# Kernel tuning notes

Hardware: AMD Instinct MI355X
Metric: run time of the kernel (lower is better)

The kernel has to match this reference:

```python
import jax, jax.numpy as jnp
import numpy as np

EMBED_DIM = 384
NUM_HEADS = 6
HEAD_DIM = EMBED_DIM // NUM_HEADS
SCALE = HEAD_DIM ** -0.5


def setup_inputs() -> dict:
    key = jax.random.key(0)
    k_x, k_qkv_w, k_qkv_b, k_p_w, k_p_b = jax.random.split(key, 5)
    B, N, C = 8, 2048, EMBED_DIM
    x = jax.random.normal(k_x, (B, N, C), dtype=jnp.float32)
    # nn.Linear init ~ U(-1/sqrt(fan_in), 1/sqrt(fan_in)); scaled normal is fine for a reference
    s = 1.0 / np.sqrt(C)
    qkv_w = jax.random.uniform(k_qkv_w, (C, 3 * C), minval=-s, maxval=s, dtype=jnp.float32)
    qkv_b = jax.random.uniform(k_qkv_b, (3 * C,), minval=-s, maxval=s, dtype=jnp.float32)
    proj_w = jax.random.uniform(k_p_w, (C, C), minval=-s, maxval=s, dtype=jnp.float32)
    proj_b = jax.random.uniform(k_p_b, (C,), minval=-s, maxval=s, dtype=jnp.float32)
    return {"x": x, "qkv_w": qkv_w, "qkv_b": qkv_b, "proj_w": proj_w, "proj_b": proj_b}


def reference(x, qkv_w, qkv_b, proj_w, proj_b):
    B, N, C = x.shape
    H, D = NUM_HEADS, C // NUM_HEADS
    qkv = x @ qkv_w + qkv_b                      # [B, N, 3C]
    qkv = qkv.reshape(B, N, 3, H, D)
    q = qkv[:, :, 0].transpose(0, 2, 1, 3)       # [B, H, N, D]
    k = qkv[:, :, 1].transpose(0, 2, 1, 3)
    v = qkv[:, :, 2].transpose(0, 2, 1, 3)
    attn = jnp.einsum('bhnd,bhmd->bhnm', q, k) * SCALE  # [B, H, N, N]
    attn = jax.nn.softmax(attn, axis=-1)
    out = jnp.einsum('bhnm,bhmd->bhnd', attn, v)        # [B, H, N, D]
    out = out.transpose(0, 2, 1, 3).reshape(B, N, C)
    return out @ proj_w + proj_b
```

## Files before the change

### kernel.cpp

```cpp
#include <hip/hip_runtime.h>
#include <hip/hip_bf16.h>
#include <stdint.h>

#define NUM_HEADS 6
#define HEAD_DIM  64
#define EMB       384
#define SEQ       2048
#define NBATCH    8
#define NBH       48
#define QKV_COLS  1152
#define ROWS      16384
#define L2E       1.44269504f

typedef __attribute__((ext_vector_type(8))) short bf16x8;
typedef __attribute__((ext_vector_type(4))) short bf16x4;
typedef __attribute__((ext_vector_type(4))) float f32x4;

typedef const __attribute__((address_space(1))) void gas_void;
typedef __attribute__((address_space(3))) void las_void;

static __device__ __forceinline__ short f2bf(float f) {
    __hip_bfloat16 h = __float2bfloat16(f);
    return __builtin_bit_cast(short, h);
}

__global__ void xcvt_kernel(const float* __restrict__ in, short* __restrict__ out) {
    int i = (blockIdx.x * 256 + threadIdx.x) * 8;
    f32x4 a = *(const f32x4*)&in[i];
    f32x4 b = *(const f32x4*)&in[i + 4];
    bf16x8 o;
    o[0] = f2bf(a[0]); o[1] = f2bf(a[1]); o[2] = f2bf(a[2]); o[3] = f2bf(a[3]);
    o[4] = f2bf(b[0]); o[5] = f2bf(b[1]); o[6] = f2bf(b[2]); o[7] = f2bf(b[3]);
    *(bf16x8*)&out[i] = o;
}

__global__ void wtrans_kernel(const float* __restrict__ in, short* __restrict__ out,
                              int rows, int cols) {
    __shared__ float tile[32][33];
    int c0 = blockIdx.x * 32, r0 = blockIdx.y * 32;
    int x = threadIdx.x, y = threadIdx.y;
#pragma unroll
    for (int i = 0; i < 32; i += 8)
        tile[y + i][x] = in[(size_t)(r0 + y + i) * cols + c0 + x];
    __syncthreads();
#pragma unroll
    for (int i = 0; i < 32; i += 8)
        out[(size_t)(c0 + y + i) * rows + r0 + x] = f2bf(tile[x][y + i]);
}

#define BM 128
#define BN 128
#define BK 64
#define LDP 80

__global__ __launch_bounds__(256, 2) void qkv_gemm_kernel(
    const short* __restrict__ Xb, const short* __restrict__ WT,
    const float* __restrict__ bias,
    short* __restrict__ Qb, short* __restrict__ Kb, short* __restrict__ Vt)
{
    __shared__ short At[BM][LDP];
    __shared__ short Bt[BN][LDP];
    const int orig = blockIdx.x;
    const int wgid = (orig & 7) * 144 + (orig >> 3);
    const int m0 = (wgid / 9) * BM;
    const int n0 = (wgid % 9) * BN;
    const int tid = threadIdx.x;
    const int lane = tid & 63, wid = tid >> 6;
    const int wm = wid >> 1, wn = wid & 1;
    const int lr = lane & 15, lg = lane >> 4;
    f32x4 acc[4][4] = {};

    for (int k0 = 0; k0 < EMB; k0 += BK) {
        int r = tid >> 3, c = (tid & 7) * 8;
#pragma unroll
        for (int i = 0; i < 4; ++i)
            *(bf16x8*)&At[r + i * 32][c] = *(const bf16x8*)&Xb[(size_t)(m0 + r + i * 32) * EMB + k0 + c];
#pragma unroll
        for (int i = 0; i < 4; ++i)
            *(bf16x8*)&Bt[r + i * 32][c] = *(const bf16x8*)&WT[(size_t)(n0 + r + i * 32) * EMB + k0 + c];
        __syncthreads();
#pragma unroll
        for (int kk = 0; kk < 2; ++kk) {
            bf16x8 af[4], bg[4];
#pragma unroll
            for (int mi = 0; mi < 4; ++mi)
                af[mi] = *(const bf16x8*)&At[wm * 64 + mi * 16 + lr][kk * 32 + lg * 8];
#pragma unroll
            for (int ni = 0; ni < 4; ++ni)
                bg[ni] = *(const bf16x8*)&Bt[wn * 64 + ni * 16 + lr][kk * 32 + lg * 8];
#pragma unroll
            for (int mi = 0; mi < 4; ++mi)
#pragma unroll
                for (int ni = 0; ni < 4; ++ni)
                    acc[mi][ni] = __builtin_amdgcn_mfma_f32_16x16x32_bf16(af[mi], bg[ni], acc[mi][ni], 0, 0, 0);
        }
        __syncthreads();
    }
    const int mat = n0 / EMB;
#pragma unroll
    for (int ni = 0; ni < 4; ++ni) {
        int col = n0 + wn * 64 + ni * 16 + lr;
        float bv = bias[col];
        int rem = col - mat * EMB;
        int h = rem >> 6, d = rem & 63;
#pragma unroll
        for (int mi = 0; mi < 4; ++mi) {
#pragma unroll
            for (int j = 0; j < 4; ++j) {
                int row = m0 + wm * 64 + mi * 16 + lg * 4 + j;
                int b = row >> 11, n = row & 2047;
                float v = acc[mi][ni][j] + bv;
                size_t bh = (size_t)(b * NUM_HEADS + h);
                if (mat == 0)      Qb[(bh * SEQ + n) * HEAD_DIM + d] = f2bf(v * (0.125f * L2E));
                else if (mat == 1) Kb[(bh * SEQ + n) * HEAD_DIM + d] = f2bf(v);
                else               Vt[(bh * HEAD_DIM + d) * SEQ + n] = f2bf(v);
            }
        }
    }
}

__global__ __launch_bounds__(256, 4) void attn_kernel(
    const short* __restrict__ Qb, const short* __restrict__ Kb,
    const short* __restrict__ Vg, short* __restrict__ AO)
{
    __shared__ alignas(16) char Kl[2][8192];
    __shared__ alignas(16) char Vl[2][8192];
    __shared__ alignas(16) char Pl[4][2048];

    const int orig = blockIdx.x;
    const int wgid = (orig & 7) * 96 + (orig >> 3);
    const int bh = wgid >> 4;
    const int qb = wgid & 15;
    const int tid = threadIdx.x, lane = tid & 63, wid = tid >> 6;
    const int lr = lane & 15, lg = lane >> 4;
    const int q0 = qb * 128 + wid * 32;
    const short* Qh = Qb + (size_t)bh * SEQ * HEAD_DIM;
    const char*  Khc = (const char*)(Kb + (size_t)bh * SEQ * HEAD_DIM);
    const char*  Vhc = (const char*)(Vg + (size_t)bh * HEAD_DIM * SEQ);

    const int s_r0 = wid * 16 + (lane >> 3);
    const int s_cb0 = ((lane & 7) * 16) ^ ((s_r0 & 7) << 4);
    const int s_r1 = s_r0 + 8;
    const int s_cb1 = ((lane & 7) * 16) ^ ((s_r1 & 7) << 4);

#define STAGE(buf, kbase)                                                               \
    do {                                                                                \
        __builtin_amdgcn_global_load_lds(                                               \
            (gas_void*)(Khc + ((size_t)(kbase) + s_r0) * 128 + s_cb0),                  \
            (las_void*)(&Kl[buf][wid * 2048]), 16, 0, 0);                               \
        __builtin_amdgcn_global_load_lds(                                               \
            (gas_void*)(Khc + ((size_t)(kbase) + s_r1) * 128 + s_cb1),                  \
            (las_void*)(&Kl[buf][wid * 2048 + 1024]), 16, 0, 0);                        \
        __builtin_amdgcn_global_load_lds(                                               \
            (gas_void*)(Vhc + (size_t)s_r0 * (SEQ * 2) + (size_t)(kbase) * 2 + s_cb0),  \
            (las_void*)(&Vl[buf][wid * 2048]), 16, 0, 0);                               \
        __builtin_amdgcn_global_load_lds(                                               \
            (gas_void*)(Vhc + (size_t)s_r1 * (SEQ * 2) + (size_t)(kbase) * 2 + s_cb1),  \
            (las_void*)(&Vl[buf][wid * 2048 + 1024]), 16, 0, 0);                        \
    } while (0)

    bf16x8 qf[2][2];
#pragma unroll
    for (int c2 = 0; c2 < 2; ++c2)
#pragma unroll
        for (int kk = 0; kk < 2; ++kk)
            qf[c2][kk] = *(const bf16x8*)&Qh[(size_t)(q0 + c2 * 16 + lr) * HEAD_DIM + kk * 32 + lg * 8];

    bf16x8 ones;
#pragma unroll
    for (int e = 0; e < 8; ++e) ones[e] = (short)0x3F80;

    f32x4 acc[2][4] = {};
    f32x4 accl[2] = {};

    char* const PlW = Pl[wid];
    const int swp = (lr & 7) << 4;

    STAGE(0, 0);
    __syncthreads();

    for (int t = 0; t < SEQ / 64; ++t) {
        const int cur = t & 1;
        if (t + 1 < SEQ / 64) STAGE(cur ^ 1, (t + 1) * 64);

        const char* Kt = Kl[cur];
        const char* Vt_ = Vl[cur];

        f32x4 s[2][4] = {};
        __builtin_amdgcn_s_setprio(1);
#pragma unroll
        for (int c = 0; c < 4; ++c) {
            const int row = c * 16 + lr;
            const int sw = (row & 7) << 4;
            bf16x8 k0 = *(const bf16x8*)(Kt + row * 128 + ((lg * 16) ^ sw));
            bf16x8 k1 = *(const bf16x8*)(Kt + row * 128 + ((64 + lg * 16) ^ sw));
            s[0][c] = __builtin_amdgcn_mfma_f32_16x16x32_bf16(k0, qf[0][0], s[0][c], 0, 0, 0);
            s[0][c] = __builtin_amdgcn_mfma_f32_16x16x32_bf16(k1, qf[0][1], s[0][c], 0, 0, 0);
            s[1][c] = __builtin_amdgcn_mfma_f32_16x16x32_bf16(k0, qf[1][0], s[1][c], 0, 0, 0);
            s[1][c] = __builtin_amdgcn_mfma_f32_16x16x32_bf16(k1, qf[1][1], s[1][c], 0, 0, 0);
        }
        __builtin_amdgcn_s_setprio(0);

        bf16x8 pb[2][2];
#pragma unroll
        for (int c2 = 0; c2 < 2; ++c2) {
#pragma unroll
            for (int c = 0; c < 4; ++c) {
                bf16x4 q4;
#pragma unroll
                for (int j = 0; j < 4; ++j)
                    q4[j] = f2bf(__builtin_amdgcn_exp2f(s[c2][c][j]));
                *(bf16x4*)(PlW + lr * 128 + ((c * 32 + lg * 8) ^ swp)) = q4;
            }
#pragma unroll
            for (int kk = 0; kk < 2; ++kk)
                pb[c2][kk] = *(const bf16x8*)(PlW + lr * 128 + ((kk * 64 + lg * 16) ^ swp));
        }

        __builtin_amdgcn_s_setprio(1);
#pragma unroll
        for (int f = 0; f < 4; ++f) {
            const int row = f * 16 + lr;
            const int sw = (row & 7) << 4;
            bf16x8 v0 = *(const bf16x8*)(Vt_ + row * 128 + ((lg * 16) ^ sw));
            bf16x8 v1 = *(const bf16x8*)(Vt_ + row * 128 + ((64 + lg * 16) ^ sw));
            acc[0][f] = __builtin_amdgcn_mfma_f32_16x16x32_bf16(v0, pb[0][0], acc[0][f], 0, 0, 0);
            acc[0][f] = __builtin_amdgcn_mfma_f32_16x16x32_bf16(v1, pb[0][1], acc[0][f], 0, 0, 0);
            acc[1][f] = __builtin_amdgcn_mfma_f32_16x16x32_bf16(v0, pb[1][0], acc[1][f], 0, 0, 0);
            acc[1][f] = __builtin_amdgcn_mfma_f32_16x16x32_bf16(v1, pb[1][1], acc[1][f], 0, 0, 0);
        }
        accl[0] = __builtin_amdgcn_mfma_f32_16x16x32_bf16(ones, pb[0][0], accl[0], 0, 0, 0);
        accl[0] = __builtin_amdgcn_mfma_f32_16x16x32_bf16(ones, pb[0][1], accl[0], 0, 0, 0);
        accl[1] = __builtin_amdgcn_mfma_f32_16x16x32_bf16(ones, pb[1][0], accl[1], 0, 0, 0);
        accl[1] = __builtin_amdgcn_mfma_f32_16x16x32_bf16(ones, pb[1][1], accl[1], 0, 0, 0);
        __builtin_amdgcn_s_setprio(0);

        __syncthreads();
    }
#undef STAGE

    const int b = bh / NUM_HEADS, h = bh - b * NUM_HEADS;
#pragma unroll
    for (int c2 = 0; c2 < 2; ++c2) {
        const float inv = 1.f / accl[c2][0];
        const size_t rowbase = ((size_t)(b * SEQ + q0 + c2 * 16 + lr)) * EMB + h * HEAD_DIM;
#pragma unroll
        for (int f = 0; f < 4; ++f) {
            bf16x4 o4;
#pragma unroll
            for (int j = 0; j < 4; ++j)
                o4[j] = f2bf(acc[c2][f][j] * inv);
            *(bf16x4*)&AO[rowbase + f * 16 + lg * 4] = o4;
        }
    }
}

__global__ __launch_bounds__(256, 2) void proj_gemm_kernel(
    const short* __restrict__ Ain, const short* __restrict__ WT,
    const float* __restrict__ bias, float* __restrict__ Out)
{
    __shared__ short At[64][LDP];
    __shared__ short Bt[128][LDP];
    const int orig = blockIdx.x;
    const int idx = orig >> 3;
    const int m0 = ((orig & 7) * 32 + idx / 3) * 64;
    const int n0 = (idx % 3) * 128;
    const int tid = threadIdx.x;
    const int lane = tid & 63, wid = tid >> 6;
    const int wm = wid >> 1, wn = wid & 1;
    const int lr = lane & 15, lg = lane >> 4;
    f32x4 acc[2][4] = {};

    for (int k0 = 0; k0 < EMB; k0 += BK) {
        int r = tid >> 3, c = (tid & 7) * 8;
#pragma unroll
        for (int i = 0; i < 2; ++i)
            *(bf16x8*)&At[r + i * 32][c] = *(const bf16x8*)&Ain[(size_t)(m0 + r + i * 32) * EMB + k0 + c];
#pragma unroll
        for (int i = 0; i < 4; ++i)
            *(bf16x8*)&Bt[r + i * 32][c] = *(const bf16x8*)&WT[(size_t)(n0 + r + i * 32) * EMB + k0 + c];
        __syncthreads();
#pragma unroll
        for (int kk = 0; kk < 2; ++kk) {
            bf16x8 af[2], bg[4];
#pragma unroll
            for (int mi = 0; mi < 2; ++mi)
                af[mi] = *(const bf16x8*)&At[wm * 32 + mi * 16 + lr][kk * 32 + lg * 8];
#pragma unroll
            for (int ni = 0; ni < 4; ++ni)
                bg[ni] = *(const bf16x8*)&Bt[wn * 64 + ni * 16 + lr][kk * 32 + lg * 8];
#pragma unroll
            for (int mi = 0; mi < 2; ++mi)
#pragma unroll
                for (int ni = 0; ni < 4; ++ni)
                    acc[mi][ni] = __builtin_amdgcn_mfma_f32_16x16x32_bf16(af[mi], bg[ni], acc[mi][ni], 0, 0, 0);
        }
        __syncthreads();
    }
#pragma unroll
    for (int ni = 0; ni < 4; ++ni) {
        int col = n0 + wn * 64 + ni * 16 + lr;
        float bv = bias[col];
#pragma unroll
        for (int mi = 0; mi < 2; ++mi)
#pragma unroll
            for (int j = 0; j < 4; ++j) {
                int row = m0 + wm * 32 + mi * 16 + lg * 4 + j;
                Out[(size_t)row * EMB + col] = acc[mi][ni][j] + bv;
            }
    }
}

extern "C" void kernel_launch(void* const* d_in, const int* in_sizes, int n_in,
                              void* d_out, int out_size, void* d_ws, size_t ws_size,
                              hipStream_t stream) {
    const float* x      = (const float*)d_in[0];
    const float* qkv_w  = (const float*)d_in[1];
    const float* qkv_b  = (const float*)d_in[2];
    const float* proj_w = (const float*)d_in[3];
    const float* proj_b = (const float*)d_in[4];
    float* out = (float*)d_out;

    char* ws = (char*)d_ws;
    short* qkv_wT  = (short*)(ws);
    short* proj_wT = (short*)(ws + 884736);
    short* Qb      = (short*)(ws + 1179648);
    short* Kb      = (short*)(ws + 13762560);
    short* Vt      = (short*)(ws + 26345472);
    short* AOXb    = (short*)(ws + 38928384);

    wtrans_kernel<<<dim3(QKV_COLS / 32, EMB / 32), dim3(32, 8), 0, stream>>>(qkv_w, qkv_wT, EMB, QKV_COLS);
    wtrans_kernel<<<dim3(EMB / 32, EMB / 32), dim3(32, 8), 0, stream>>>(proj_w, proj_wT, EMB, EMB);
    xcvt_kernel<<<dim3(ROWS * EMB / 8 / 256), 256, 0, stream>>>(x, AOXb);
    qkv_gemm_kernel<<<dim3(ROWS / BM * (QKV_COLS / BN)), 256, 0, stream>>>(AOXb, qkv_wT, qkv_b, Qb, Kb, Vt);
    attn_kernel<<<dim3(NBH * (SEQ / 128)), 256, 0, stream>>>(Qb, Kb, Vt, AOXb);
    proj_gemm_kernel<<<dim3(ROWS / 64 * (EMB / 128)), 256, 0, stream>>>(AOXb, proj_wT, proj_b, out);
}
```

Measured before the change: 138.4 us.

## Double-buffer GEMM tiles via direct global-to-LDS loads with XOR swizzle

Both the QKV and projection GEMMs now load tiles with global_load_lds into double-buffered, XOR-swizzled shared memory, prefetching the next K-tile while MFMAs run on the current one. Wave priority is raised around the MFMA loop. The V output, previously written with strided scalar stores into the transposed Vt, is now transposed through LDS and written as contiguous 16-byte vectors. The proj kernel's occupancy hint rises to 3; the larger LDS footprint and the extra barrier in the V epilogue are the trade-offs.

```diff
diff --git a/kernel.cpp b/kernel.cpp
--- a/kernel.cpp
+++ b/kernel.cpp
@@ -51,15 +51,13 @@
 #define BM 128
 #define BN 128
 #define BK 64
-#define LDP 80
 
 __global__ __launch_bounds__(256, 2) void qkv_gemm_kernel(
     const short* __restrict__ Xb, const short* __restrict__ WT,
     const float* __restrict__ bias,
     short* __restrict__ Qb, short* __restrict__ Kb, short* __restrict__ Vt)
 {
-    __shared__ short At[BM][LDP];
-    __shared__ short Bt[BN][LDP];
+    __shared__ alignas(16) char smem[2][32768];
     const int orig = blockIdx.x;
     const int wgid = (orig & 7) * 144 + (orig >> 3);
     const int m0 = (wgid / 9) * BM;
@@ -68,54 +66,105 @@
     const int lane = tid & 63, wid = tid >> 6;
     const int wm = wid >> 1, wn = wid & 1;
     const int lr = lane & 15, lg = lane >> 4;
+    const char* Xc = (const char*)Xb;
+    const char* Wc = (const char*)WT;
+
+    const int t_r = wid * 32 + (lane >> 3);
+    const int t_cb = ((lane & 7) * 16) ^ (((lane >> 3) & 7) << 4);
+
+#define GSTAGE(buf, k0)                                                                     \
+    do {                                                                                    \
+        _Pragma("unroll") for (int i = 0; i < 4; ++i)                                       \
+            __builtin_amdgcn_global_load_lds(                                               \
+                (gas_void*)(Xc + ((size_t)(m0 + t_r + i * 8)) * (EMB * 2) + (k0) * 2 + t_cb), \
+                (las_void*)(&smem[buf][wid * 4096 + i * 1024]), 16, 0, 0);                  \
+        _Pragma("unroll") for (int i = 0; i < 4; ++i)                                       \
+            __builtin_amdgcn_global_load_lds(                                               \
+                (gas_void*)(Wc + ((size_t)(n0 + t_r + i * 8)) * (EMB * 2) + (k0) * 2 + t_cb), \
+                (las_void*)(&smem[buf][16384 + wid * 4096 + i * 1024]), 16, 0, 0);          \
+    } while (0)
+
     f32x4 acc[4][4] = {};
 
-    for (int k0 = 0; k0 < EMB; k0 += BK) {
-        int r = tid >> 3, c = (tid & 7) * 8;
-#pragma unroll
-        for (int i = 0; i < 4; ++i)
-            *(bf16x8*)&At[r + i * 32][c] = *(const bf16x8*)&Xb[(size_t)(m0 + r + i * 32) * EMB + k0 + c];
-#pragma unroll
-        for (int i = 0; i < 4; ++i)
-            *(bf16x8*)&Bt[r + i * 32][c] = *(const bf16x8*)&WT[(size_t)(n0 + r + i * 32) * EMB + k0 + c];
-        __syncthreads();
+    GSTAGE(0, 0);
+    __syncthreads();
+    for (int t = 0; t < EMB / BK; ++t) {
+        const int cur = t & 1;
+        if (t + 1 < EMB / BK) GSTAGE(cur ^ 1, (t + 1) * BK);
+        const char* Ab = smem[cur];
+        const char* Bb = smem[cur] + 16384;
+        __builtin_amdgcn_s_setprio(1);
 #pragma unroll
         for (int kk = 0; kk < 2; ++kk) {
             bf16x8 af[4], bg[4];
 #pragma unroll
-            for (int mi = 0; mi < 4; ++mi)
-                af[mi] = *(const bf16x8*)&At[wm * 64 + mi * 16 + lr][kk * 32 + lg * 8];
-#pragma unroll
-            for (int ni = 0; ni < 4; ++ni)
-                bg[ni] = *(const bf16x8*)&Bt[wn * 64 + ni * 16 + lr][kk * 32 + lg * 8];
+            for (int mi = 0; mi < 4; ++mi) {
+                const int row = wm * 64 + mi * 16 + lr;
+                af[mi] = *(const bf16x8*)(Ab + row * 128 + ((kk * 64 + lg * 16) ^ ((row & 7) << 4)));
+            }
+#pragma unroll
+            for (int ni = 0; ni < 4; ++ni) {
+                const int row = wn * 64 + ni * 16 + lr;
+                bg[ni] = *(const bf16x8*)(Bb + row * 128 + ((kk * 64 + lg * 16) ^ ((row & 7) << 4)));
+            }
 #pragma unroll
             for (int mi = 0; mi < 4; ++mi)
 #pragma unroll
                 for (int ni = 0; ni < 4; ++ni)
                     acc[mi][ni] = __builtin_amdgcn_mfma_f32_16x16x32_bf16(af[mi], bg[ni], acc[mi][ni], 0, 0, 0);
         }
+        __builtin_amdgcn_s_setprio(0);
         __syncthreads();
     }
+#undef GSTAGE
+
     const int mat = n0 / EMB;
-#pragma unroll
-    for (int ni = 0; ni < 4; ++ni) {
-        int col = n0 + wn * 64 + ni * 16 + lr;
-        float bv = bias[col];
-        int rem = col - mat * EMB;
-        int h = rem >> 6, d = rem & 63;
-#pragma unroll
-        for (int mi = 0; mi < 4; ++mi) {
-#pragma unroll
-            for (int j = 0; j < 4; ++j) {
-                int row = m0 + wm * 64 + mi * 16 + lg * 4 + j;
-                int b = row >> 11, n = row & 2047;
-                float v = acc[mi][ni][j] + bv;
-                size_t bh = (size_t)(b * NUM_HEADS + h);
-                if (mat == 0)      Qb[(bh * SEQ + n) * HEAD_DIM + d] = f2bf(v * (0.125f * L2E));
-                else if (mat == 1) Kb[(bh * SEQ + n) * HEAD_DIM + d] = f2bf(v);
-                else               Vt[(bh * HEAD_DIM + d) * SEQ + n] = f2bf(v);
-            }
-        }
+    if (mat != 2) {
+#pragma unroll
+        for (int ni = 0; ni < 4; ++ni) {
+            int col = n0 + wn * 64 + ni * 16 + lr;
+            float bv = bias[col];
+            int rem = col - mat * EMB;
+            int h = rem >> 6, d = rem & 63;
+#pragma unroll
+            for (int mi = 0; mi < 4; ++mi) {
+#pragma unroll
+                for (int j = 0; j < 4; ++j) {
+                    int row = m0 + wm * 64 + mi * 16 + lg * 4 + j;
+                    int b = row >> 11, n = row & 2047;
+                    float v = acc[mi][ni][j] + bv;
+                    size_t bh = (size_t)(b * NUM_HEADS + h);
+                    if (mat == 0) Qb[(bh * SEQ + n) * HEAD_DIM + d] = f2bf(v * (0.125f * L2E));
+                    else          Kb[(bh * SEQ + n) * HEAD_DIM + d] = f2bf(v);
+                }
+            }
+        }
+    } else {
+        short (*Tt)[136] = (short (*)[136])&smem[0][0];
+#pragma unroll
+        for (int ni = 0; ni < 4; ++ni) {
+            int col = n0 + wn * 64 + ni * 16 + lr;
+            float bv = bias[col];
+            int c_loc = wn * 64 + ni * 16 + lr;
+#pragma unroll
+            for (int mi = 0; mi < 4; ++mi) {
+                bf16x4 o4;
+#pragma unroll
+                for (int j = 0; j < 4; ++j)
+                    o4[j] = f2bf(acc[mi][ni][j] + bv);
+                *(bf16x4*)&Tt[c_loc][wm * 64 + mi * 16 + lg * 4] = o4;
+            }
+        }
+        __syncthreads();
+        const int b = m0 >> 11, nbase = m0 & 2047;
+        const int d_loc = tid >> 1;
+        const int nn = (tid & 1) * 64;
+        const int rem = n0 - 2 * EMB + d_loc;
+        const int h = rem >> 6, d = rem & 63;
+        short* dst = Vt + ((size_t)(b * NUM_HEADS + h) * HEAD_DIM + d) * SEQ + nbase + nn;
+#pragma unroll
+        for (int e = 0; e < 8; ++e)
+            *(bf16x8*)&dst[e * 8] = *(const bf16x8*)&Tt[d_loc][nn + e * 8];
     }
 }
 
@@ -255,12 +304,11 @@
     }
 }
 
-__global__ __launch_bounds__(256, 2) void proj_gemm_kernel(
+__global__ __launch_bounds__(256, 3) void proj_gemm_kernel(
     const short* __restrict__ Ain, const short* __restrict__ WT,
     const float* __restrict__ bias, float* __restrict__ Out)
 {
-    __shared__ short At[64][LDP];
-    __shared__ short Bt[128][LDP];
+    __shared__ alignas(16) char smem[2][24576];
     const int orig = blockIdx.x;
     const int idx = orig >> 3;
     const int m0 = ((orig & 7) * 32 + idx / 3) * 64;
@@ -269,34 +317,59 @@
     const int lane = tid & 63, wid = tid >> 6;
     const int wm = wid >> 1, wn = wid & 1;
     const int lr = lane & 15, lg = lane >> 4;
+    const char* Ac = (const char*)Ain;
+    const char* Wc = (const char*)WT;
+
+    const int a_r = wid * 16 + (lane >> 3);
+    const int b_r = wid * 32 + (lane >> 3);
+    const int t_cb = ((lane & 7) * 16) ^ (((lane >> 3) & 7) << 4);
+
+#define PSTAGE(buf, k0)                                                                     \
+    do {                                                                                    \
+        _Pragma("unroll") for (int i = 0; i < 2; ++i)                                       \
+            __builtin_amdgcn_global_load_lds(                                               \
+                (gas_void*)(Ac + ((size_t)(m0 + a_r + i * 8)) * (EMB * 2) + (k0) * 2 + t_cb), \
+                (las_void*)(&smem[buf][wid * 2048 + i * 1024]), 16, 0, 0);                  \
+        _Pragma("unroll") for (int i = 0; i < 4; ++i)                                       \
+            __builtin_amdgcn_global_load_lds(                                               \
+                (gas_void*)(Wc + ((size_t)(n0 + b_r + i * 8)) * (EMB * 2) + (k0) * 2 + t_cb), \
+                (las_void*)(&smem[buf][8192 + wid * 4096 + i * 1024]), 16, 0, 0);           \
+    } while (0)
+
     f32x4 acc[2][4] = {};
 
-    for (int k0 = 0; k0 < EMB; k0 += BK) {
-        int r = tid >> 3, c = (tid & 7) * 8;
-#pragma unroll
-        for (int i = 0; i < 2; ++i)
-            *(bf16x8*)&At[r + i * 32][c] = *(const bf16x8*)&Ain[(size_t)(m0 + r + i * 32) * EMB + k0 + c];
-#pragma unroll
-        for (int i = 0; i < 4; ++i)
-            *(bf16x8*)&Bt[r + i * 32][c] = *(const bf16x8*)&WT[(size_t)(n0 + r + i * 32) * EMB + k0 + c];
-        __syncthreads();
+    PSTAGE(0, 0);
+    __syncthreads();
+    for (int t = 0; t < EMB / BK; ++t) {
+        const int cur = t & 1;
+        if (t + 1 < EMB / BK) PSTAGE(cur ^ 1, (t + 1) * BK);
+        const char* Ab = smem[cur];
+        const char* Bb = smem[cur] + 8192;
+        __builtin_amdgcn_s_setprio(1);
 #pragma unroll
         for (int kk = 0; kk < 2; ++kk) {
             bf16x8 af[2], bg[4];
 #pragma unroll
-            for (int mi = 0; mi < 2; ++mi)
-                af[mi] = *(const bf16x8*)&At[wm * 32 + mi * 16 + lr][kk * 32 + lg * 8];
-#pragma unroll
-            for (int ni = 0; ni < 4; ++ni)
-                bg[ni] = *(const bf16x8*)&Bt[wn * 64 + ni * 16 + lr][kk * 32 + lg * 8];
+            for (int mi = 0; mi < 2; ++mi) {
+                const int row = wm * 32 + mi * 16 + lr;
+                af[mi] = *(const bf16x8*)(Ab + row * 128 + ((kk * 64 + lg * 16) ^ ((row & 7) << 4)));
+            }
+#pragma unroll
+            for (int ni = 0; ni < 4; ++ni) {
+                const int row = wn * 64 + ni * 16 + lr;
+                bg[ni] = *(const bf16x8*)(Bb + row * 128 + ((kk * 64 + lg * 16) ^ ((row & 7) << 4)));
+            }
 #pragma unroll
             for (int mi = 0; mi < 2; ++mi)
 #pragma unroll
                 for (int ni = 0; ni < 4; ++ni)
                     acc[mi][ni] = __builtin_amdgcn_mfma_f32_16x16x32_bf16(af[mi], bg[ni], acc[mi][ni], 0, 0, 0);
         }
+        __builtin_amdgcn_s_setprio(0);
         __syncthreads();
     }
+#undef PSTAGE
+
 #pragma unroll
     for (int ni = 0; ni < 4; ++ni) {
         int col = n0 + wn * 64 + ni * 16 + lr;
```

New measurement: 119.8 us. 13.4% less time.
